# Kernel optimization log

Hardware: AMD Instinct MI355X
Metric: run time of the kernel (lower is better)

Reference implementation:

```python
import jax, jax.numpy as jnp
import numpy as np

D = 768; H = 12; DH = 64; P = 16; G = 14; NP = 196; L = 197
LD = 4; GD = 12          # local / latent depths
RL = 12; RG = 8          # tokens merged per layer (total_merge // depth)
B = 8
EPS = 1e-6


def layernorm(x, g, b):
    mu = x.mean(-1, keepdims=True)
    v = ((x - mu) ** 2).mean(-1, keepdims=True)
    return (x - mu) / jnp.sqrt(v + EPS) * g + b


def attention(x, size, qkv_w, qkv_b, pw, pb):
    # proportional attention: logits += log(token size)
    Bn, N, _ = x.shape
    qkv = (x @ qkv_w + qkv_b).reshape(Bn, N, 3, H, DH)
    q, k, v = (qkv[:, :, i].transpose(0, 2, 1, 3) for i in range(3))  # bhnd
    logits = jnp.einsum('bhqd,bhkd->bhqk', q, k) * (DH ** -0.5)
    logits = logits + jnp.log(size)[:, None, None, :, 0]
    a = jax.nn.softmax(logits, axis=-1)
    o = jnp.einsum('bhqk,bhkd->bhqd', a, v).transpose(0, 2, 1, 3).reshape(Bn, N, D)
    return o @ pw + pb, k.mean(1)  # metric = mean key over heads


def tome_merge(x, size, metric, r, tok_map):
    # ToMe bipartite soft matching + weighted-average merge + source-map update
    Bn, N, _ = x.shape
    t1, t2 = (N + 1) // 2, N // 2
    m = metric / jnp.linalg.norm(metric, axis=-1, keepdims=True)
    scores = jnp.einsum('bid,bjd->bij', m[:, ::2], m[:, 1::2])
    scores = scores.at[:, 0, :].set(-jnp.inf)  # protect cls token
    node_max, node_idx = scores.max(-1), scores.argmax(-1).astype(jnp.int32)
    order = jnp.argsort(-node_max, axis=-1).astype(jnp.int32)
    src_idx = order[:, :r]
    unm_idx = jnp.sort(order[:, r:], axis=-1)  # cls stays first
    dst_idx = jnp.take_along_axis(node_idx, src_idx, axis=1)
    bi = jnp.arange(Bn)[:, None]

    def merge_sum(v):
        a, b = v[:, ::2], v[:, 1::2]
        unm = jnp.take_along_axis(a, unm_idx[..., None], axis=1)
        s = jnp.take_along_axis(a, src_idx[..., None], axis=1)
        b = b.at[bi, dst_idx].add(s)
        return jnp.concatenate([unm, b], axis=1)

    new_size = merge_sum(size)
    new_x = merge_sum(x * size) / new_size
    # per-step old->new index map, then compose with running source map
    pos_a = jnp.zeros((Bn, t1), jnp.int32)
    pos_a = pos_a.at[bi, unm_idx].set(jnp.arange(t1 - r, dtype=jnp.int32))
    pos_a = pos_a.at[bi, src_idx].set((t1 - r) + dst_idx)
    step = jnp.zeros((Bn, N), jnp.int32)
    step = step.at[:, ::2].set(pos_a)
    step = step.at[:, 1::2].set((t1 - r) + jnp.arange(t2, dtype=jnp.int32)[None])
    return new_x, new_size, jnp.take_along_axis(step, tok_map, axis=1)


def encode(x, size, tok_map, r, p):
    ln1g, ln1b, qw, qb, pw, pb, ln2g, ln2b, f1w, f1b, f2w, f2b = p
    for i in range(ln1g.shape[0]):
        a, metric = attention(layernorm(x, ln1g[i], ln1b[i]), size, qw[i], qb[i], pw[i], pb[i])
        x = x + a
        if r > 0:
            x, size, tok_map = tome_merge(x, size, metric, r, tok_map)
        h = layernorm(x, ln2g[i], ln2b[i])
        x = x + (jax.nn.gelu(h @ f1w[i] + f1b[i], approximate=False) @ f2w[i] + f2b[i])
    return x, size, tok_map


def setup_inputs() -> dict:
    key = jax.random.key(0)
    ks = iter(jax.random.split(key, 64))
    def w(shape):
        return jax.random.normal(next(ks), shape, jnp.float32) * 0.02
    def blocks(d, pre):
        return {pre + 'ln1g': jnp.ones((d, D)), pre + 'ln1b': jnp.zeros((d, D)),
                pre + 'qkv_w': w((d, D, 3 * D)), pre + 'qkv_b': jnp.zeros((d, 3 * D)),
                pre + 'proj_w': w((d, D, D)), pre + 'proj_b': jnp.zeros((d, D)),
                pre + 'ln2g': jnp.ones((d, D)), pre + 'ln2b': jnp.zeros((d, D)),
                pre + 'fc1w': w((d, D, 4 * D)), pre + 'fc1b': jnp.zeros((d, 4 * D)),
                pre + 'fc2w': w((d, 4 * D, D)), pre + 'fc2b': jnp.zeros((d, D))}
    inp = dict(x=jax.random.normal(next(ks), (B, 3, 224, 224), jnp.float32),
               patch_w=w((3 * P * P, D)), patch_b=jnp.zeros((D,)),
               cls_tok=w((1, 1, D)), pos_emb=w((1, L, D)),
               l_ng=jnp.ones((D,)), l_nb=jnp.zeros((D,)),
               g_ng=jnp.ones((D,)), g_nb=jnp.zeros((D,)),
               head_w=w((D, 10)), head_b=jnp.zeros((10,)))
    inp.update(blocks(LD, 'l_'))
    inp.update(blocks(GD, 'g_'))
    return inp


def reference(x, patch_w, patch_b, cls_tok, pos_emb,
              l_ln1g, l_ln1b, l_qkv_w, l_qkv_b, l_proj_w, l_proj_b,
              l_ln2g, l_ln2b, l_fc1w, l_fc1b, l_fc2w, l_fc2b, l_ng, l_nb,
              g_ln1g, g_ln1b, g_qkv_w, g_qkv_b, g_proj_w, g_proj_b,
              g_ln2g, g_ln2b, g_fc1w, g_fc1b, g_fc2w, g_fc2b, g_ng, g_nb,
              head_w, head_b):
    Bn = x.shape[0]
    # non-overlapping 16x16 patchify == conv stride 16
    patches = x.reshape(Bn, 3, G, P, G, P).transpose(0, 2, 4, 1, 3, 5).reshape(Bn, NP, 3 * P * P)
    t = patches @ patch_w + patch_b
    t = jnp.concatenate([jnp.broadcast_to(cls_tok, (Bn, 1, D)), t], axis=1) + pos_emb
    size = jnp.ones((Bn, L, 1), t.dtype)
    tmap = jnp.broadcast_to(jnp.arange(L, dtype=jnp.int32)[None], (Bn, L))  # token_map_for_dtem
    lp = (l_ln1g, l_ln1b, l_qkv_w, l_qkv_b, l_proj_w, l_proj_b, l_ln2g, l_ln2b, l_fc1w, l_fc1b, l_fc2w, l_fc2b)
    xl, size, tmap = encode(t, size, tmap, RL, lp)   # local encoder: 197 -> 149 tokens
    xl = layernorm(xl, l_ng, l_nb)
    N1 = xl.shape[1]
    smap = jnp.broadcast_to(jnp.arange(N1, dtype=jnp.int32)[None], (Bn, N1))  # latent source_map
    gp = (g_ln1g, g_ln1b, g_qkv_w, g_qkv_b, g_proj_w, g_proj_b, g_ln2g, g_ln2b, g_fc1w, g_fc1b, g_fc2w, g_fc2b)
    xg, size, smap = encode(xl, size, smap, RG, gp)  # latent encoder: 149 -> 53 tokens
    xg = layernorm(xg, g_ng, g_nb)
    xr = jnp.take_along_axis(xg, smap[..., None], axis=1)   # token_unmerge_from_map (ToMe)
    xf = jnp.take_along_axis(xr, tmap[..., None], axis=1)   # token_unmerge_from_map_for_dtem
    return xf[:, 0] @ head_w + head_b  # cls token -> logits (B, 10)
```

## Files before the change

kernel.cpp:

```cpp
#include <hip/hip_runtime.h>
#include <math.h>

#define NB 8
#define SD 768
#define NHEAD 12
#define LMAX 197
#define QBLK 32
#define KBLK 64

typedef __attribute__((ext_vector_type(8))) short bf16x8;
typedef __attribute__((ext_vector_type(4))) float f32x4;

static __device__ __forceinline__ float geluf(float x){
    return 0.5f*x*(1.0f+erff(x*0.70710678118654752440f));
}

static __device__ __forceinline__ void split_bf16(float v, ushort& h, ushort& l){
    uint u = __float_as_uint(v);
    uint hb = (u + 0x7FFFu + ((u>>16)&1u)) >> 16;
    h = (ushort)hb;
    float rem = v - __uint_as_float(hb<<16);
    uint u2 = __float_as_uint(rem);
    l = (ushort)((u2 + 0x7FFFu + ((u2>>16)&1u)) >> 16);
}

__global__ __launch_bounds__(256) void wconv(const float* __restrict__ W,
        ushort* __restrict__ Hi, ushort* __restrict__ Lo, int K, int Nc)
{
    __shared__ float tile[32][33];
    int z = blockIdx.z;
    const float* Wz = W + (size_t)z*K*Nc;
    ushort* Hz = Hi + (size_t)z*Nc*K;
    ushort* Lz = Lo + (size_t)z*Nc*K;
    int n0 = blockIdx.x*32, k0 = blockIdx.y*32;
    int tx = threadIdx.x&31, ty = threadIdx.x>>5;
    #pragma unroll
    for (int i=0;i<32;i+=8) tile[ty+i][tx] = Wz[(size_t)(k0+ty+i)*Nc + n0+tx];
    __syncthreads();
    #pragma unroll
    for (int i=0;i<32;i+=8){
        float v = tile[tx][ty+i];
        ushort h,l; split_bf16(v,h,l);
        size_t o = (size_t)(n0+ty+i)*K + k0+tx;
        Hz[o]=h; Lz[o]=l;
    }
}

template<int EPI>
__global__ __launch_bounds__(256) void gemm_mfma(const ushort* __restrict__ AHi,
        const ushort* __restrict__ ALo, const ushort* __restrict__ WHi,
        const ushort* __restrict__ WLo, const float* __restrict__ bias,
        const float* __restrict__ R, float* __restrict__ C,
        ushort* __restrict__ CHi, ushort* __restrict__ CLo,
        int M, int Nc, int K, int ntok)
{
    __shared__ ushort sAhi[64*64], sAlo[64*64], sBhi[64*64], sBlo[64*64];
    const int t = threadIdx.x;
    const int bx = blockIdx.x, by = blockIdx.y;
    const int w = t>>6, l = t&63, lr = l&15, lg = l>>4;
    const int wr = w>>1, wc = w&1;
    const int srow = t>>3;
    const int kbyte = (t&7)*16;

    f32x4 acc[2][2];
    #pragma unroll
    for (int i=0;i<2;i++)
        #pragma unroll
        for (int j=0;j<2;j++) acc[i][j] = (f32x4){0.f,0.f,0.f,0.f};

    for (int k0=0;k0<K;k0+=64){
        #pragma unroll
        for (int p=0;p<2;p++){
            int row = p*32 + srow;
            int ar = by*64 + row; if (ar >= M) ar = M-1;
            int b = ar/ntok; int n = ar - b*ntok;
            size_t ga = ((size_t)(b*LMAX+n)*K + k0)*2 + kbyte;
            uint4 vah = *(const uint4*)((const char*)AHi + ga);
            uint4 val = *(const uint4*)((const char*)ALo + ga);
            uint off = (uint)((row*128 + kbyte) ^ ((row&7)<<4));
            *(uint4*)((char*)sAhi + off) = vah;
            *(uint4*)((char*)sAlo + off) = val;
            size_t gw = ((size_t)(bx*64+row)*K + k0)*2 + kbyte;
            uint4 vwh = *(const uint4*)((const char*)WHi + gw);
            uint4 vwl = *(const uint4*)((const char*)WLo + gw);
            *(uint4*)((char*)sBhi + off) = vwh;
            *(uint4*)((char*)sBlo + off) = vwl;
        }
        __syncthreads();
        #pragma unroll
        for (int kk=0;kk<2;kk++){
            bf16x8 ah[2], al[2], bh[2], bl[2];
            #pragma unroll
            for (int m=0;m<2;m++){
                int row = wr*32 + m*16 + lr;
                uint off = (uint)((row*128 + kk*64 + lg*16) ^ ((row&7)<<4));
                ah[m] = *(bf16x8*)((char*)sAhi + off);
                al[m] = *(bf16x8*)((char*)sAlo + off);
            }
            #pragma unroll
            for (int n=0;n<2;n++){
                int col = wc*32 + n*16 + lr;
                uint off = (uint)((col*128 + kk*64 + lg*16) ^ ((col&7)<<4));
                bh[n] = *(bf16x8*)((char*)sBhi + off);
                bl[n] = *(bf16x8*)((char*)sBlo + off);
            }
            #pragma unroll
            for (int m=0;m<2;m++)
                #pragma unroll
                for (int n=0;n<2;n++){
                    acc[m][n] = __builtin_amdgcn_mfma_f32_16x16x32_bf16(ah[m], bh[n], acc[m][n], 0,0,0);
                    acc[m][n] = __builtin_amdgcn_mfma_f32_16x16x32_bf16(ah[m], bl[n], acc[m][n], 0,0,0);
                    acc[m][n] = __builtin_amdgcn_mfma_f32_16x16x32_bf16(al[m], bh[n], acc[m][n], 0,0,0);
                }
        }
        __syncthreads();
    }
    #pragma unroll
    for (int m=0;m<2;m++){
        #pragma unroll
        for (int n=0;n<2;n++){
            int gcol = bx*64 + wc*32 + n*16 + lr;
            float bv = bias[gcol];
            #pragma unroll
            for (int r=0;r<4;r++){
                int grow = by*64 + wr*32 + m*16 + lg*4 + r;
                if (grow >= M) continue;
                int b = grow/ntok; int ni = grow - b*ntok;
                size_t off = (size_t)(b*LMAX+ni)*Nc + gcol;
                float v = acc[m][n][r] + bv;
                if (EPI==1){
                    v = geluf(v);
                    ushort h,lo; split_bf16(v,h,lo);
                    CHi[off]=h; CLo[off]=lo;
                } else {
                    if (EPI==2) v += R[off];
                    C[off] = v;
                }
            }
        }
    }
}

__device__ __forceinline__ float block_sum256(float v){
    __shared__ float red[4];
    for (int o=32;o>0;o>>=1) v += __shfl_down(v,o,64);
    int t=threadIdx.x;
    if ((t&63)==0) red[t>>6]=v;
    __syncthreads();
    float r = red[0]+red[1]+red[2]+red[3];
    __syncthreads();
    return r;
}

__global__ __launch_bounds__(256) void ln_split(const float* __restrict__ X,
        const float* __restrict__ gam, const float* __restrict__ bet,
        ushort* __restrict__ YHi, ushort* __restrict__ YLo)
{
    int n = blockIdx.x, b = blockIdx.y, t = threadIdx.x;
    const float* xr = X + ((size_t)(b*LMAX+n))*SD;
    size_t ro = ((size_t)(b*LMAX+n))*SD;
    float v0=xr[t], v1=xr[t+256], v2=xr[t+512];
    float mu = block_sum256(v0+v1+v2) * (1.0f/768.0f);
    float d0=v0-mu, d1=v1-mu, d2=v2-mu;
    float var = block_sum256(d0*d0+d1*d1+d2*d2) * (1.0f/768.0f);
    float rs = rsqrtf(var + 1e-6f);
    float y0 = d0*rs*gam[t]     + bet[t];
    float y1 = d1*rs*gam[t+256] + bet[t+256];
    float y2 = d2*rs*gam[t+512] + bet[t+512];
    ushort h,lo;
    split_bf16(y0,h,lo); YHi[ro+t]=h;     YLo[ro+t]=lo;
    split_bf16(y1,h,lo); YHi[ro+t+256]=h; YLo[ro+t+256]=lo;
    split_bf16(y2,h,lo); YHi[ro+t+512]=h; YLo[ro+t+512]=lo;
}

__global__ __launch_bounds__(256) void ln_kernel(const float* __restrict__ X,
        const float* __restrict__ gam, const float* __restrict__ bet,
        float* __restrict__ Y)
{
    int n = blockIdx.x, b = blockIdx.y, t = threadIdx.x;
    const float* xr = X + ((size_t)(b*LMAX+n))*SD;
    float* yr = Y + ((size_t)(b*LMAX+n))*SD;
    float v0=xr[t], v1=xr[t+256], v2=xr[t+512];
    float mu = block_sum256(v0+v1+v2) * (1.0f/768.0f);
    float d0=v0-mu, d1=v1-mu, d2=v2-mu;
    float var = block_sum256(d0*d0+d1*d1+d2*d2) * (1.0f/768.0f);
    float rs = rsqrtf(var + 1e-6f);
    yr[t]     = d0*rs*gam[t]     + bet[t];
    yr[t+256] = d1*rs*gam[t+256] + bet[t+256];
    yr[t+512] = d2*rs*gam[t+512] + bet[t+512];
}

__global__ __launch_bounds__(256) void attn_tile(const float* __restrict__ QKV,
        const float* __restrict__ SZ, ushort* __restrict__ OHi,
        ushort* __restrict__ OLo, int N)
{
    const int q0 = blockIdx.x*QBLK;
    const int h = blockIdx.y, b = blockIdx.z, t = threadIdx.x;
    __shared__ float Qs[QBLK][68];
    __shared__ float KVs[KBLK][68];
    __shared__ float Ls[QBLK][200];
    __shared__ float szl[KBLK];
    __shared__ float invs[QBLK];

    {
        int row = t>>3, seg = t&7;
        int q = q0 + row;
        if (q < N){
            const float* src = QKV + ((size_t)(b*LMAX+q))*2304 + h*64 + seg*8;
            *(float4*)&Qs[row][seg*8]   = *(const float4*)src;
            *(float4*)&Qs[row][seg*8+4] = *(const float4*)(src+4);
        } else {
            float4 z = make_float4(0.f,0.f,0.f,0.f);
            *(float4*)&Qs[row][seg*8]   = z;
            *(float4*)&Qs[row][seg*8+4] = z;
        }
    }
    const int tq = t>>3, tk = t&7;
    const int nkt = (N+KBLK-1)/KBLK;

    for (int kt=0; kt<nkt; ++kt){
        int kbase = kt*KBLK;
        __syncthreads();
        {
            int row = t>>2, seg = t&3;
            int ktok = kbase + row;
            float4 a,b4,c,d4;
            if (ktok < N){
                const float* src = QKV + ((size_t)(b*LMAX+ktok))*2304 + 768 + h*64 + seg*16;
                a=*(const float4*)src; b4=*(const float4*)(src+4);
                c=*(const float4*)(src+8); d4=*(const float4*)(src+12);
            } else {
                a=b4=c=d4=make_float4(0.f,0.f,0.f,0.f);
            }
            *(float4*)&KVs[row][seg*16]   =a;
            *(float4*)&KVs[row][seg*16+4] =b4;
            *(float4*)&KVs[row][seg*16+8] =c;
            *(float4*)&KVs[row][seg*16+12]=d4;
            if (t < KBLK){
                int kk2 = kbase + t;
                szl[t] = (kk2<N) ? logf(SZ[b*LMAX+kk2]) : 0.f;
            }
        }
        __syncthreads();
        float acc[8];
        #pragma unroll
        for (int j=0;j<8;j++) acc[j]=0.f;
        #pragma unroll 4
        for (int d4=0; d4<16; ++d4){
            float4 qv = *(const float4*)&Qs[tq][d4*4];
            #pragma unroll
            for (int j=0;j<8;j++){
                float4 kv = *(const float4*)&KVs[tk+8*j][d4*4];
                acc[j] += qv.x*kv.x + qv.y*kv.y + qv.z*kv.z + qv.w*kv.w;
            }
        }
        #pragma unroll
        for (int j=0;j<8;j++){
            int kk = kbase + tk + 8*j;
            if (kk < N) Ls[tq][kk] = acc[j]*0.125f + szl[tk+8*j];
        }
    }
    __syncthreads();

    {
        float m = -INFINITY;
        for (int k=tk;k<N;k+=8) m = fmaxf(m, Ls[tq][k]);
        #pragma unroll
        for (int o=1;o<8;o<<=1) m = fmaxf(m, __shfl_xor(m,o,64));
        float s = 0.f;
        for (int k=tk;k<N;k+=8){
            float p = expf(Ls[tq][k]-m);
            Ls[tq][k]=p; s+=p;
        }
        #pragma unroll
        for (int o=1;o<8;o<<=1) s += __shfl_xor(s,o,64);
        if (tk==0) invs[tq] = 1.0f/s;
    }

    float o0[8];
    #pragma unroll
    for (int i=0;i<8;i++) o0[i]=0.f;
    for (int kt=0; kt<nkt; ++kt){
        int kbase = kt*KBLK;
        __syncthreads();
        {
            int row = t>>2, seg = t&3;
            int ktok = kbase + row;
            float4 a,b4,c,d4;
            if (ktok < N){
                const float* src = QKV + ((size_t)(b*LMAX+ktok))*2304 + 1536 + h*64 + seg*16;
                a=*(const float4*)src; b4=*(const float4*)(src+4);
                c=*(const float4*)(src+8); d4=*(const float4*)(src+12);
            } else {
                a=b4=c=d4=make_float4(0.f,0.f,0.f,0.f);
            }
            *(float4*)&KVs[row][seg*16]   =a;
            *(float4*)&KVs[row][seg*16+4] =b4;
            *(float4*)&KVs[row][seg*16+8] =c;
            *(float4*)&KVs[row][seg*16+12]=d4;
        }
        __syncthreads();
        int kmax = N - kbase; if (kmax > KBLK) kmax = KBLK;
        for (int kk=0; kk<kmax; ++kk){
            float p = Ls[tq][kbase+kk];
            float4 v0 = *(const float4*)&KVs[kk][tk*8];
            float4 v1 = *(const float4*)&KVs[kk][tk*8+4];
            o0[0]+=p*v0.x; o0[1]+=p*v0.y; o0[2]+=p*v0.z; o0[3]+=p*v0.w;
            o0[4]+=p*v1.x; o0[5]+=p*v1.y; o0[6]+=p*v1.z; o0[7]+=p*v1.w;
        }
    }
    int q = q0 + tq;
    if (q < N){
        float inv = invs[tq];
        ushort hh[8], ll[8];
        #pragma unroll
        for (int i=0;i<8;i++){ split_bf16(o0[i]*inv, hh[i], ll[i]); }
        size_t o = ((size_t)(b*LMAX+q))*SD + h*64 + tk*8;
        *(ushort4*)(OHi+o)   = make_ushort4(hh[0],hh[1],hh[2],hh[3]);
        *(ushort4*)(OHi+o+4) = make_ushort4(hh[4],hh[5],hh[6],hh[7]);
        *(ushort4*)(OLo+o)   = make_ushort4(ll[0],ll[1],ll[2],ll[3]);
        *(ushort4*)(OLo+o+4) = make_ushort4(ll[4],ll[5],ll[6],ll[7]);
    }
}

__global__ void metric_k(const float* __restrict__ QKV, float* __restrict__ MET)
{
    const int n = blockIdx.x, b = blockIdx.y, d = threadIdx.x;
    const float* base = QKV + ((size_t)(b*LMAX+n))*2304 + 768 + d;
    float s=0.f;
    #pragma unroll
    for (int h=0;h<12;h++) s += base[h*64];
    s *= (1.0f/12.0f);
    float sq = s*s;
    for (int o=32;o>0;o>>=1) sq += __shfl_down(sq,o,64);
    float nrm = sqrtf(__shfl(sq,0,64));
    MET[((size_t)(b*LMAX+n))*64 + d] = s/nrm;
}

__global__ __launch_bounds__(128) void scores_k(const float* __restrict__ MET,
        float* __restrict__ NMAX, int* __restrict__ NIDX, int t2)
{
    const int i = blockIdx.x, b = blockIdx.y, t = threadIdx.x;
    __shared__ float ma[64];
    __shared__ float vals[128];
    __shared__ int idxs[128];
    if (t<64) ma[t] = MET[((size_t)(b*LMAX+2*i))*64+t];
    __syncthreads();
    float val = -INFINITY;
    if (t<t2 && i>0){
        const float* mb = MET + ((size_t)(b*LMAX+2*t+1))*64;
        float dot=0.f;
        #pragma unroll 8
        for (int dd=0;dd<64;dd++) dot += ma[dd]*mb[dd];
        val = dot;
    }
    vals[t]=val; idxs[t]=t; __syncthreads();
    for (int s=64;s>0;s>>=1){
        if (t<s){
            float v2=vals[t+s], v1=vals[t]; int i2=idxs[t+s];
            if (v2>v1 || (v2==v1 && i2<idxs[t])){ vals[t]=v2; idxs[t]=i2; }
        }
        __syncthreads();
    }
    if (t==0){ NMAX[b*128+i]=vals[0]; NIDX[b*128+i]=idxs[0]; }
}

__global__ __launch_bounds__(128) void plan_k(const float* __restrict__ NMAX,
        const int* __restrict__ NIDX, int* __restrict__ SRC, int* __restrict__ DST,
        int* __restrict__ STEP, int* __restrict__ INV, int t1, int t2, int r)
{
    const int b = blockIdx.x, i = threadIdx.x;
    __shared__ float nm[128];
    __shared__ int issrc[128];
    nm[i] = (i<t1) ? NMAX[b*128+i] : INFINITY;
    __syncthreads();
    int rank=0, is=0, ni=0;
    if (i<t1){
        float m = nm[i];
        for (int j=0;j<t1;j++){ float a=nm[j]; if (a>m || (a==m && j<i)) rank++; }
        is = (rank<r) ? 1:0;
        ni = NIDX[b*128+i];
    }
    issrc[i]=is; __syncthreads();
    if (i<t1){
        if (is){ SRC[b*16+rank]=i; DST[b*16+rank]=ni; STEP[b*LMAX+2*i] = t1-r+ni; }
        else {
            int cnt=0;
            for (int j=0;j<i;j++) cnt += 1-issrc[j];
            STEP[b*LMAX+2*i]=cnt;
            INV[b*LMAX+cnt]=2*i;
        }
    }
    if (i<t2){ STEP[b*LMAX+2*i+1]=t1-r+i; INV[b*LMAX+(t1-r)+i]=2*i+1; }
}

__global__ __launch_bounds__(256) void merge_fused(const float* __restrict__ X,
        const float* __restrict__ SZ, const int* __restrict__ INV,
        const int* __restrict__ SRC, const int* __restrict__ DST,
        float* __restrict__ XO, float* __restrict__ SZO, int t1, int r)
{
    int p = blockIdx.x, b = blockIdx.y, t = threadIdx.x;
    int base = t1 - r;
    float acc0, acc1, acc2, snew;
    if (p < base){
        int tok = INV[b*LMAX+p];
        float s = SZ[b*LMAX+tok];
        const float* xr = X + (size_t)(b*LMAX+tok)*SD;
        acc0=xr[t]*s; acc1=xr[t+256]*s; acc2=xr[t+512]*s; snew=s;
    } else {
        int d = p - base;
        int tok = 2*d+1;
        float s = SZ[b*LMAX+tok];
        const float* xr = X + (size_t)(b*LMAX+tok)*SD;
        acc0=xr[t]*s; acc1=xr[t+256]*s; acc2=xr[t+512]*s; snew=s;
        for (int k=0;k<r;k++){
            if (DST[b*16+k]==d){
                int st = 2*SRC[b*16+k];
                float ss = SZ[b*LMAX+st];
                const float* xs = X + (size_t)(b*LMAX+st)*SD;
                acc0+=xs[t]*ss; acc1+=xs[t+256]*ss; acc2+=xs[t+512]*ss; snew+=ss;
            }
        }
    }
    float inv = 1.0f/snew;
    float* o = XO + (size_t)(b*LMAX+p)*SD;
    o[t]=acc0*inv; o[t+256]=acc1*inv; o[t+512]=acc2*inv;
    if (t==0) SZO[b*LMAX+p]=snew;
}

__global__ void map_upd(int* __restrict__ MAP, const int* __restrict__ STEP, int mlen)
{
    int i = blockIdx.x*256+threadIdx.x;
    if (i >= NB*mlen) return;
    int b=i/mlen, t=i-b*mlen;
    MAP[b*LMAX+t] = STEP[b*LMAX + MAP[b*LMAX+t]];
}

__global__ void patchify(const float* __restrict__ X, ushort* __restrict__ PHi,
        ushort* __restrict__ PLo)
{
    size_t i = (size_t)blockIdx.x*256 + threadIdx.x;
    if (i >= (size_t)NB*196*768) return;
    int f = i % 768; size_t q = i/768; int p = q % 196; int b = q/196;
    int c = f >> 8, py = (f>>4)&15, px = f&15;
    int gy = p/14, gx = p - gy*14;
    float v = X[(((size_t)b*3 + c)*224 + gy*16+py)*224 + gx*16+px];
    ushort h,l; split_bf16(v,h,l);
    size_t o = ((size_t)(b*LMAX+p))*768 + f;
    PHi[o]=h; PLo[o]=l;
}

__global__ void assemble(const float* __restrict__ T, const float* __restrict__ cls,
        const float* __restrict__ pos, float* __restrict__ Xo)
{
    size_t i = (size_t)blockIdx.x*256 + threadIdx.x;
    if (i >= (size_t)NB*LMAX*768) return;
    int d = i % 768; size_t q = i/768; int n = q % LMAX; int b = q/LMAX;
    float v = (n==0) ? cls[d] : T[((size_t)(b*LMAX+n-1))*768+d];
    Xo[((size_t)(b*LMAX+n))*768+d] = v + pos[n*768+d];
}

__global__ void init_state(float* __restrict__ SZ, int* __restrict__ TMAP, int* __restrict__ SMAP)
{
    int i = blockIdx.x*256+threadIdx.x;
    if (i >= NB*LMAX) return;
    SZ[i]=1.0f;
    int n=i%LMAX;
    TMAP[i]=n;
    if (n<149) SMAP[i]=n;
}

__global__ void head_k(const float* __restrict__ XG, const int* __restrict__ SMAP,
        const int* __restrict__ TMAP, const float* __restrict__ HW,
        const float* __restrict__ HB, float* __restrict__ OUT)
{
    int t = threadIdx.x;
    if (t>=80) return;
    int b=t/10, o=t-b*10;
    int row = SMAP[b*LMAX + TMAP[b*LMAX]];
    const float* xr = XG + ((size_t)(b*LMAX+row))*SD;
    float acc = HB[o];
    for (int d=0;d<SD;d++) acc += xr[d]*HW[d*10+o];
    OUT[b*10+o]=acc;
}

extern "C" void kernel_launch(void* const* d_in, const int* in_sizes, int n_in,
                              void* d_out, int out_size, void* d_ws, size_t ws_size,
                              hipStream_t stream)
{
    const float* x_in    = (const float*)d_in[0];
    const float* patch_w = (const float*)d_in[1];
    const float* patch_b = (const float*)d_in[2];
    const float* cls     = (const float*)d_in[3];
    const float* pos     = (const float*)d_in[4];
    const float* l_ng    = (const float*)d_in[5];
    const float* l_nb    = (const float*)d_in[6];
    const float* g_ng    = (const float*)d_in[7];
    const float* g_nb    = (const float*)d_in[8];
    const float* head_w  = (const float*)d_in[9];
    const float* head_b  = (const float*)d_in[10];
    const float* L[12];  for (int i=0;i<12;i++) L[i]  = (const float*)d_in[11+i];
    const float* Gp[12]; for (int i=0;i<12;i++) Gp[i] = (const float*)d_in[23+i];
    float* out = (float*)d_out;

    float* fp = (float*)d_ws;
    float* xA      = fp; fp += (size_t)NB*LMAX*SD;
    float* xB      = fp; fp += (size_t)NB*LMAX*SD;
    float* qkvbuf  = fp; fp += (size_t)NB*LMAX*2304;
    float* metricbuf=fp; fp += (size_t)NB*LMAX*64;
    float* szA     = fp; fp += NB*LMAX;
    float* szB     = fp; fp += NB*LMAX;
    float* nodemax = fp; fp += NB*128;
    int* ip = (int*)fp;
    int* tmap    = ip; ip += NB*LMAX;
    int* smap    = ip; ip += NB*LMAX;
    int* stepbuf = ip; ip += NB*LMAX;
    int* invrow  = ip; ip += NB*LMAX;
    int* nodeidx = ip; ip += NB*128;
    int* srcs    = ip; ip += NB*16;
    int* dsts    = ip; ip += NB*16;
    uintptr_t up = ((uintptr_t)ip + 15) & ~(uintptr_t)15;
    ushort* sp = (ushort*)up;
    ushort* lnHi = sp; sp += (size_t)NB*LMAX*SD;
    ushort* lnLo = sp; sp += (size_t)NB*LMAX*SD;
    ushort* oHi  = sp; sp += (size_t)NB*LMAX*SD;
    ushort* oLo  = sp; sp += (size_t)NB*LMAX*SD;
    ushort* hHi  = sp; sp += (size_t)NB*LMAX*3072;
    ushort* hLo  = sp; sp += (size_t)NB*LMAX*3072;
    ushort* pHi  = sp; sp += (size_t)NB*LMAX*SD;
    ushort* pLo  = sp; sp += (size_t)NB*LMAX*SD;
    ushort* patchHi = sp; sp += (size_t)768*768;
    ushort* patchLo = sp; sp += (size_t)768*768;
    ushort* qkvHi = sp; sp += (size_t)4*768*2304;
    ushort* qkvLo = sp; sp += (size_t)4*768*2304;
    ushort* projHi= sp; sp += (size_t)4*768*768;
    ushort* projLo= sp; sp += (size_t)4*768*768;
    ushort* fc1Hi = sp; sp += (size_t)4*768*3072;
    ushort* fc1Lo = sp; sp += (size_t)4*768*3072;
    ushort* fc2Hi = sp; sp += (size_t)4*3072*768;
    ushort* fc2Lo = sp; sp += (size_t)4*3072*768;

    float *xc = xA, *xn = xB, *szc = szA, *szn = szB;

    auto conv_chunk = [&](const float* qw, const float* pw, const float* f1w,
                          const float* f2w, int nz)
    {
        wconv<<<dim3(2304/32,768/32,nz),256,0,stream>>>(qw, qkvHi, qkvLo, SD, 2304);
        wconv<<<dim3(768/32,768/32,nz),256,0,stream>>>(pw, projHi, projLo, SD, SD);
        wconv<<<dim3(3072/32,768/32,nz),256,0,stream>>>(f1w, fc1Hi, fc1Lo, SD, 3072);
        wconv<<<dim3(768/32,3072/32,nz),256,0,stream>>>(f2w, fc2Hi, fc2Lo, 3072, SD);
    };

    auto run_block = [&](const float* ln1g, const float* ln1b, const float* qb,
                         const float* pb, const float* ln2g, const float* ln2b,
                         const float* f1b, const float* f2b,
                         int slot, int N, int r, int* mp, int mlen)
    {
        int M = NB*N;
        const ushort* qH = qkvHi + (size_t)slot*768*2304;
        const ushort* qL = qkvLo + (size_t)slot*768*2304;
        const ushort* pH = projHi + (size_t)slot*768*768;
        const ushort* pL = projLo + (size_t)slot*768*768;
        const ushort* f1H = fc1Hi + (size_t)slot*768*3072;
        const ushort* f1L = fc1Lo + (size_t)slot*768*3072;
        const ushort* f2H = fc2Hi + (size_t)slot*3072*768;
        const ushort* f2L = fc2Lo + (size_t)slot*3072*768;

        ln_split<<<dim3(N,NB),256,0,stream>>>(xc, ln1g, ln1b, lnHi, lnLo);
        gemm_mfma<0><<<dim3(2304/64,(M+63)/64),256,0,stream>>>(lnHi, lnLo, qH, qL, qb, nullptr, qkvbuf, nullptr, nullptr, M, 2304, SD, N);
        attn_tile<<<dim3((N+QBLK-1)/QBLK,NHEAD,NB),256,0,stream>>>(qkvbuf, szc, oHi, oLo, N);
        metric_k<<<dim3(N,NB),64,0,stream>>>(qkvbuf, metricbuf);
        gemm_mfma<2><<<dim3(SD/64,(M+63)/64),256,0,stream>>>(oHi, oLo, pH, pL, pb, xc, xc, nullptr, nullptr, M, SD, SD, N);
        int t1=(N+1)/2, t2=N/2, Nn=N-r;
        scores_k<<<dim3(t1,NB),128,0,stream>>>(metricbuf, nodemax, nodeidx, t2);
        plan_k<<<NB,128,0,stream>>>(nodemax, nodeidx, srcs, dsts, stepbuf, invrow, t1, t2, r);
        merge_fused<<<dim3(Nn,NB),256,0,stream>>>(xc, szc, invrow, srcs, dsts, xn, szn, t1, r);
        map_upd<<<(NB*mlen+255)/256,256,0,stream>>>(mp, stepbuf, mlen);
        int M2 = NB*Nn;
        ln_split<<<dim3(Nn,NB),256,0,stream>>>(xn, ln2g, ln2b, lnHi, lnLo);
        gemm_mfma<1><<<dim3(3072/64,(M2+63)/64),256,0,stream>>>(lnHi, lnLo, f1H, f1L, f1b, nullptr, nullptr, hHi, hLo, M2, 3072, SD, Nn);
        gemm_mfma<2><<<dim3(SD/64,(M2+63)/64),256,0,stream>>>(hHi, hLo, f2H, f2L, f2b, xn, xn, nullptr, nullptr, M2, SD, 3072, Nn);
        float* tf; tf=xc; xc=xn; xn=tf; tf=szc; szc=szn; szn=tf;
    };

    {
        int tot = NB*196*768;
        patchify<<<(tot+255)/256,256,0,stream>>>(x_in, pHi, pLo);
        wconv<<<dim3(768/32,768/32,1),256,0,stream>>>(patch_w, patchHi, patchLo, SD, SD);
        gemm_mfma<0><<<dim3(SD/64,(NB*196+63)/64),256,0,stream>>>(pHi, pLo, patchHi, patchLo, patch_b, nullptr, qkvbuf, nullptr, nullptr, NB*196, SD, SD, 196);
        int tot2 = NB*LMAX*768;
        assemble<<<(tot2+255)/256,256,0,stream>>>(qkvbuf, cls, pos, xc);
        init_state<<<(NB*LMAX+255)/256,256,0,stream>>>(szc, tmap, smap);
    }

    conv_chunk(L[2], L[4], L[8], L[10], 4);
    int N = 197;
    for (int i=0;i<4;i++){
        run_block(L[0]+i*768, L[1]+i*768, L[3]+(size_t)i*2304,
                  L[5]+(size_t)i*768, L[6]+i*768, L[7]+i*768,
                  L[9]+(size_t)i*3072, L[11]+(size_t)i*768,
                  i, N, 12, tmap, 197);
        N -= 12;
    }
    ln_kernel<<<dim3(N,NB),256,0,stream>>>(xc, l_ng, l_nb, xc);

    for (int c=0;c<3;c++){
        conv_chunk(Gp[2]+(size_t)(4*c)*768*2304, Gp[4]+(size_t)(4*c)*768*768,
                   Gp[8]+(size_t)(4*c)*768*3072, Gp[10]+(size_t)(4*c)*3072*768, 4);
        for (int j=0;j<4;j++){
            int i = 4*c+j;
            run_block(Gp[0]+i*768, Gp[1]+i*768, Gp[3]+(size_t)i*2304,
                      Gp[5]+(size_t)i*768, Gp[6]+i*768, Gp[7]+i*768,
                      Gp[9]+(size_t)i*3072, Gp[11]+(size_t)i*768,
                      j, N, 8, smap, 149);
            N -= 8;
        }
    }
    ln_kernel<<<dim3(N,NB),256,0,stream>>>(xc, g_ng, g_nb, qkvbuf);
    head_k<<<1,128,0,stream>>>(qkvbuf, smap, tmap, head_w, head_b, out);
}
```

Measured before the change: 3.294 ms.

## Split-K the narrow projection and FC2 GEMMs and register-prefetch the next K tile

The proj and fc2 GEMMs, whose output is only 768 wide, now split K four ways across blockIdx.z. Each slice writes fp32 partials to a new workspace buffer, and a separate reduce kernel adds bias and the residual. This puts more blocks on the GPU for these small grids. All GEMMs also load the next K tile into registers while the current one is used, so global-load latency overlaps with MFMA work. The cost is extra partial-sum traffic, one more kernel launch per GEMM, and a change in summation order.

```diff
diff --git a/kernel.cpp b/kernel.cpp
--- a/kernel.cpp
+++ b/kernel.cpp
@@ -46,13 +46,13 @@
     }
 }
 
-template<int EPI>
+template<int EPI, int SPLITK>
 __global__ __launch_bounds__(256) void gemm_mfma(const ushort* __restrict__ AHi,
         const ushort* __restrict__ ALo, const ushort* __restrict__ WHi,
         const ushort* __restrict__ WLo, const float* __restrict__ bias,
         const float* __restrict__ R, float* __restrict__ C,
         ushort* __restrict__ CHi, ushort* __restrict__ CLo,
-        int M, int Nc, int K, int ntok)
+        float* __restrict__ Part, int M, int Nc, int K, int ntok)
 {
     __shared__ ushort sAhi[64*64], sAlo[64*64], sBhi[64*64], sBlo[64*64];
     const int t = threadIdx.x;
@@ -62,29 +62,53 @@
     const int srow = t>>3;
     const int kbyte = (t&7)*16;
 
+    const int Ks = K/SPLITK;
+    const int kbeg = blockIdx.z*Ks;
+
+    size_t gaB[2], gwB[2];
+    #pragma unroll
+    for (int p=0;p<2;p++){
+        int row = p*32 + srow;
+        int ar = by*64 + row; if (ar >= M) ar = M-1;
+        int b = ar/ntok; int n = ar - b*ntok;
+        gaB[p] = ((size_t)(b*LMAX+n)*K)*2 + kbyte;
+        gwB[p] = ((size_t)(bx*64+row)*K)*2 + kbyte;
+    }
+
+    uint4 rah[2], ral[2], rwh[2], rwl[2];
+    #pragma unroll
+    for (int p=0;p<2;p++){
+        rah[p] = *(const uint4*)((const char*)AHi + gaB[p] + (size_t)kbeg*2);
+        ral[p] = *(const uint4*)((const char*)ALo + gaB[p] + (size_t)kbeg*2);
+        rwh[p] = *(const uint4*)((const char*)WHi + gwB[p] + (size_t)kbeg*2);
+        rwl[p] = *(const uint4*)((const char*)WLo + gwB[p] + (size_t)kbeg*2);
+    }
+
     f32x4 acc[2][2];
     #pragma unroll
     for (int i=0;i<2;i++)
         #pragma unroll
         for (int j=0;j<2;j++) acc[i][j] = (f32x4){0.f,0.f,0.f,0.f};
 
-    for (int k0=0;k0<K;k0+=64){
+    for (int k0=kbeg; k0<kbeg+Ks; k0+=64){
         #pragma unroll
         for (int p=0;p<2;p++){
             int row = p*32 + srow;
-            int ar = by*64 + row; if (ar >= M) ar = M-1;
-            int b = ar/ntok; int n = ar - b*ntok;
-            size_t ga = ((size_t)(b*LMAX+n)*K + k0)*2 + kbyte;
-            uint4 vah = *(const uint4*)((const char*)AHi + ga);
-            uint4 val = *(const uint4*)((const char*)ALo + ga);
             uint off = (uint)((row*128 + kbyte) ^ ((row&7)<<4));
-            *(uint4*)((char*)sAhi + off) = vah;
-            *(uint4*)((char*)sAlo + off) = val;
-            size_t gw = ((size_t)(bx*64+row)*K + k0)*2 + kbyte;
-            uint4 vwh = *(const uint4*)((const char*)WHi + gw);
-            uint4 vwl = *(const uint4*)((const char*)WLo + gw);
-            *(uint4*)((char*)sBhi + off) = vwh;
-            *(uint4*)((char*)sBlo + off) = vwl;
+            *(uint4*)((char*)sAhi + off) = rah[p];
+            *(uint4*)((char*)sAlo + off) = ral[p];
+            *(uint4*)((char*)sBhi + off) = rwh[p];
+            *(uint4*)((char*)sBlo + off) = rwl[p];
+        }
+        if (k0+64 < kbeg+Ks){
+            size_t ko = (size_t)(k0+64)*2;
+            #pragma unroll
+            for (int p=0;p<2;p++){
+                rah[p] = *(const uint4*)((const char*)AHi + gaB[p] + ko);
+                ral[p] = *(const uint4*)((const char*)ALo + gaB[p] + ko);
+                rwh[p] = *(const uint4*)((const char*)WHi + gwB[p] + ko);
+                rwl[p] = *(const uint4*)((const char*)WLo + gwB[p] + ko);
+            }
         }
         __syncthreads();
         #pragma unroll
@@ -115,30 +139,71 @@
         }
         __syncthreads();
     }
-    #pragma unroll
-    for (int m=0;m<2;m++){
-        #pragma unroll
-        for (int n=0;n<2;n++){
-            int gcol = bx*64 + wc*32 + n*16 + lr;
-            float bv = bias[gcol];
+
+    if (SPLITK > 1){
+        float* Pz = Part + (size_t)blockIdx.z*M*Nc;
+        #pragma unroll
+        for (int m=0;m<2;m++){
             #pragma unroll
-            for (int r=0;r<4;r++){
-                int grow = by*64 + wr*32 + m*16 + lg*4 + r;
-                if (grow >= M) continue;
-                int b = grow/ntok; int ni = grow - b*ntok;
-                size_t off = (size_t)(b*LMAX+ni)*Nc + gcol;
-                float v = acc[m][n][r] + bv;
-                if (EPI==1){
-                    v = geluf(v);
-                    ushort h,lo; split_bf16(v,h,lo);
-                    CHi[off]=h; CLo[off]=lo;
-                } else {
-                    if (EPI==2) v += R[off];
-                    C[off] = v;
+            for (int n=0;n<2;n++){
+                int gcol = bx*64 + wc*32 + n*16 + lr;
+                #pragma unroll
+                for (int r=0;r<4;r++){
+                    int grow = by*64 + wr*32 + m*16 + lg*4 + r;
+                    if (grow >= M) continue;
+                    Pz[(size_t)grow*Nc + gcol] = acc[m][n][r];
                 }
             }
         }
-    }
+    } else {
+        #pragma unroll
+        for (int m=0;m<2;m++){
+            #pragma unroll
+            for (int n=0;n<2;n++){
+                int gcol = bx*64 + wc*32 + n*16 + lr;
+                float bv = bias[gcol];
+                #pragma unroll
+                for (int r=0;r<4;r++){
+                    int grow = by*64 + wr*32 + m*16 + lg*4 + r;
+                    if (grow >= M) continue;
+                    int b = grow/ntok; int ni = grow - b*ntok;
+                    size_t off = (size_t)(b*LMAX+ni)*Nc + gcol;
+                    float v = acc[m][n][r] + bv;
+                    if (EPI==1){
+                        v = geluf(v);
+                        ushort h,lo; split_bf16(v,h,lo);
+                        CHi[off]=h; CLo[off]=lo;
+                    } else {
+                        if (EPI==2) v += R[off];
+                        C[off] = v;
+                    }
+                }
+            }
+        }
+    }
+}
+
+__global__ __launch_bounds__(256) void reduce_k(const float* __restrict__ P,
+        const float* __restrict__ bias, const float* __restrict__ R,
+        float* __restrict__ C, int M, int Nc, int S, int ntok)
+{
+    int idx = blockIdx.x*256 + threadIdx.x;
+    int tot = M*(Nc/4);
+    if (idx >= tot) return;
+    int grow = idx/(Nc/4), c4 = idx - grow*(Nc/4);
+    size_t po = (size_t)grow*Nc + c4*4;
+    float4 a = *(const float4*)(P + po);
+    for (int s=1;s<S;s++){
+        float4 v = *(const float4*)(P + (size_t)s*M*Nc + po);
+        a.x+=v.x; a.y+=v.y; a.z+=v.z; a.w+=v.w;
+    }
+    int b = grow/ntok, n = grow - b*ntok;
+    size_t off = (size_t)(b*LMAX+n)*Nc + c4*4;
+    float4 bv = *(const float4*)(bias + c4*4);
+    float4 rv = *(const float4*)(R + off);
+    float4 o;
+    o.x=a.x+bv.x+rv.x; o.y=a.y+bv.y+rv.y; o.z=a.z+bv.z+rv.z; o.w=a.w+bv.w+rv.w;
+    *(float4*)(C + off) = o;
 }
 
 __device__ __forceinline__ float block_sum256(float v){
@@ -508,6 +573,7 @@
     float* xB      = fp; fp += (size_t)NB*LMAX*SD;
     float* qkvbuf  = fp; fp += (size_t)NB*LMAX*2304;
     float* metricbuf=fp; fp += (size_t)NB*LMAX*64;
+    float* partbuf = fp; fp += (size_t)4*NB*LMAX*SD;
     float* szA     = fp; fp += NB*LMAX;
     float* szB     = fp; fp += NB*LMAX;
     float* nodemax = fp; fp += NB*128;
@@ -557,6 +623,7 @@
                          int slot, int N, int r, int* mp, int mlen)
     {
         int M = NB*N;
+        int Mt = (M+63)/64;
         const ushort* qH = qkvHi + (size_t)slot*768*2304;
         const ushort* qL = qkvLo + (size_t)slot*768*2304;
         const ushort* pH = projHi + (size_t)slot*768*768;
@@ -567,19 +634,22 @@
         const ushort* f2L = fc2Lo + (size_t)slot*3072*768;
 
         ln_split<<<dim3(N,NB),256,0,stream>>>(xc, ln1g, ln1b, lnHi, lnLo);
-        gemm_mfma<0><<<dim3(2304/64,(M+63)/64),256,0,stream>>>(lnHi, lnLo, qH, qL, qb, nullptr, qkvbuf, nullptr, nullptr, M, 2304, SD, N);
+        gemm_mfma<0,1><<<dim3(2304/64,Mt),256,0,stream>>>(lnHi, lnLo, qH, qL, qb, nullptr, qkvbuf, nullptr, nullptr, nullptr, M, 2304, SD, N);
         attn_tile<<<dim3((N+QBLK-1)/QBLK,NHEAD,NB),256,0,stream>>>(qkvbuf, szc, oHi, oLo, N);
         metric_k<<<dim3(N,NB),64,0,stream>>>(qkvbuf, metricbuf);
-        gemm_mfma<2><<<dim3(SD/64,(M+63)/64),256,0,stream>>>(oHi, oLo, pH, pL, pb, xc, xc, nullptr, nullptr, M, SD, SD, N);
+        gemm_mfma<0,4><<<dim3(SD/64,Mt,4),256,0,stream>>>(oHi, oLo, pH, pL, nullptr, nullptr, nullptr, nullptr, nullptr, partbuf, M, SD, SD, N);
+        reduce_k<<<(M*(SD/4)+255)/256,256,0,stream>>>(partbuf, pb, xc, xc, M, SD, 4, N);
         int t1=(N+1)/2, t2=N/2, Nn=N-r;
         scores_k<<<dim3(t1,NB),128,0,stream>>>(metricbuf, nodemax, nodeidx, t2);
         plan_k<<<NB,128,0,stream>>>(nodemax, nodeidx, srcs, dsts, stepbuf, invrow, t1, t2, r);
         merge_fused<<<dim3(Nn,NB),256,0,stream>>>(xc, szc, invrow, srcs, dsts, xn, szn, t1, r);
         map_upd<<<(NB*mlen+255)/256,256,0,stream>>>(mp, stepbuf, mlen);
         int M2 = NB*Nn;
+        int M2t = (M2+63)/64;
         ln_split<<<dim3(Nn,NB),256,0,stream>>>(xn, ln2g, ln2b, lnHi, lnLo);
-        gemm_mfma<1><<<dim3(3072/64,(M2+63)/64),256,0,stream>>>(lnHi, lnLo, f1H, f1L, f1b, nullptr, nullptr, hHi, hLo, M2, 3072, SD, Nn);
-        gemm_mfma<2><<<dim3(SD/64,(M2+63)/64),256,0,stream>>>(hHi, hLo, f2H, f2L, f2b, xn, xn, nullptr, nullptr, M2, SD, 3072, Nn);
+        gemm_mfma<1,1><<<dim3(3072/64,M2t),256,0,stream>>>(lnHi, lnLo, f1H, f1L, f1b, nullptr, nullptr, hHi, hLo, nullptr, M2, 3072, SD, Nn);
+        gemm_mfma<0,4><<<dim3(SD/64,M2t,4),256,0,stream>>>(hHi, hLo, f2H, f2L, nullptr, nullptr, nullptr, nullptr, nullptr, partbuf, M2, SD, 3072, Nn);
+        reduce_k<<<(M2*(SD/4)+255)/256,256,0,stream>>>(partbuf, f2b, xn, xn, M2, SD, 4, Nn);
         float* tf; tf=xc; xc=xn; xn=tf; tf=szc; szc=szn; szn=tf;
     };
 
@@ -587,7 +657,7 @@
         int tot = NB*196*768;
         patchify<<<(tot+255)/256,256,0,stream>>>(x_in, pHi, pLo);
         wconv<<<dim3(768/32,768/32,1),256,0,stream>>>(patch_w, patchHi, patchLo, SD, SD);
-        gemm_mfma<0><<<dim3(SD/64,(NB*196+63)/64),256,0,stream>>>(pHi, pLo, patchHi, patchLo, patch_b, nullptr, qkvbuf, nullptr, nullptr, NB*196, SD, SD, 196);
+        gemm_mfma<0,1><<<dim3(SD/64,(NB*196+63)/64),256,0,stream>>>(pHi, pLo, patchHi, patchLo, patch_b, nullptr, qkvbuf, nullptr, nullptr, nullptr, NB*196, SD, SD, 196);
         int tot2 = NB*LMAX*768;
         assemble<<<(tot2+255)/256,256,0,stream>>>(qkvbuf, cls, pos, xc);
         init_state<<<(NB*LMAX+255)/256,256,0,stream>>>(szc, tmap, smap);
```

After: 6.808 ms. 107% more time.

## Double-buffer GEMM LDS tiles using direct global-to-LDS async loads

Applied to the files above, without the earlier changes.

The split-bf16 MFMA GEMM now keeps two LDS buffers per operand and issues global_load_lds for the next K tile while computing on the current one, so loads no longer pass through registers. The XOR swizzle moves to the global-side address, since each lane's chunk lands at a fixed LDS slot, and the per-row base pointers are hoisted out of the K loop. This is meant to hide global memory latency behind the MFMAs. In exchange it doubles shared memory per block, which may lower occupancy, and it depends on the swizzle mapping matching exactly.

```diff
diff --git a/kernel.cpp b/kernel.cpp
--- a/kernel.cpp
+++ b/kernel.cpp
@@ -10,6 +10,8 @@
 
 typedef __attribute__((ext_vector_type(8))) short bf16x8;
 typedef __attribute__((ext_vector_type(4))) float f32x4;
+typedef const __attribute__((address_space(1))) unsigned int gu32_t;
+typedef __attribute__((address_space(3))) unsigned int lu32_t;
 
 static __device__ __forceinline__ float geluf(float x){
     return 0.5f*x*(1.0f+erff(x*0.70710678118654752440f));
@@ -54,13 +56,25 @@
         ushort* __restrict__ CHi, ushort* __restrict__ CLo,
         int M, int Nc, int K, int ntok)
 {
-    __shared__ ushort sAhi[64*64], sAlo[64*64], sBhi[64*64], sBlo[64*64];
+    __shared__ ushort sAhi[2][4096], sAlo[2][4096], sBhi[2][4096], sBlo[2][4096];
     const int t = threadIdx.x;
     const int bx = blockIdx.x, by = blockIdx.y;
     const int w = t>>6, l = t&63, lr = l&15, lg = l>>4;
     const int wr = w>>1, wc = w&1;
     const int srow = t>>3;
-    const int kbyte = (t&7)*16;
+    const uint kchunk = (uint)(((l&7) ^ (l>>3)) << 4);
+
+    const char* pA[2][2]; const char* pW[2][2];
+    #pragma unroll
+    for (int p=0;p<2;p++){
+        int row = p*32 + srow;
+        int ar = by*64 + row; if (ar >= M) ar = M-1;
+        int b = ar/ntok; int n = ar - b*ntok;
+        size_t ab = ((size_t)(b*LMAX+n)*K)*2 + kchunk;
+        size_t wb = ((size_t)(bx*64+row)*K)*2 + kchunk;
+        pA[p][0] = (const char*)AHi + ab;  pA[p][1] = (const char*)ALo + ab;
+        pW[p][0] = (const char*)WHi + wb;  pW[p][1] = (const char*)WLo + wb;
+    }
 
     f32x4 acc[2][2];
     #pragma unroll
@@ -68,25 +82,31 @@
         #pragma unroll
         for (int j=0;j<2;j++) acc[i][j] = (f32x4){0.f,0.f,0.f,0.f};
 
-    for (int k0=0;k0<K;k0+=64){
+    const int nt = K/64;
+    int buf = 0;
+
+    auto stage = [&](int bf, int kt){
+        size_t ko = (size_t)kt*128;
         #pragma unroll
         for (int p=0;p<2;p++){
-            int row = p*32 + srow;
-            int ar = by*64 + row; if (ar >= M) ar = M-1;
-            int b = ar/ntok; int n = ar - b*ntok;
-            size_t ga = ((size_t)(b*LMAX+n)*K + k0)*2 + kbyte;
-            uint4 vah = *(const uint4*)((const char*)AHi + ga);
-            uint4 val = *(const uint4*)((const char*)ALo + ga);
-            uint off = (uint)((row*128 + kbyte) ^ ((row&7)<<4));
-            *(uint4*)((char*)sAhi + off) = vah;
-            *(uint4*)((char*)sAlo + off) = val;
-            size_t gw = ((size_t)(bx*64+row)*K + k0)*2 + kbyte;
-            uint4 vwh = *(const uint4*)((const char*)WHi + gw);
-            uint4 vwl = *(const uint4*)((const char*)WLo + gw);
-            *(uint4*)((char*)sBhi + off) = vwh;
-            *(uint4*)((char*)sBlo + off) = vwl;
-        }
-        __syncthreads();
+            uint lb = (uint)((p*32 + w*8)*64);
+            __builtin_amdgcn_global_load_lds((gu32_t*)(pA[p][0]+ko), (lu32_t*)&sAhi[bf][lb], 16, 0, 0);
+            __builtin_amdgcn_global_load_lds((gu32_t*)(pA[p][1]+ko), (lu32_t*)&sAlo[bf][lb], 16, 0, 0);
+            __builtin_amdgcn_global_load_lds((gu32_t*)(pW[p][0]+ko), (lu32_t*)&sBhi[bf][lb], 16, 0, 0);
+            __builtin_amdgcn_global_load_lds((gu32_t*)(pW[p][1]+ko), (lu32_t*)&sBlo[bf][lb], 16, 0, 0);
+        }
+    };
+
+    stage(0, 0);
+    asm volatile("s_waitcnt vmcnt(0)" ::: "memory");
+    __builtin_amdgcn_s_barrier();
+
+    for (int kt=0; kt<nt; ++kt){
+        if (kt+1 < nt) stage(buf^1, kt+1);
+        const char* bAhi = (const char*)&sAhi[buf][0];
+        const char* bAlo = (const char*)&sAlo[buf][0];
+        const char* bBhi = (const char*)&sBhi[buf][0];
+        const char* bBlo = (const char*)&sBlo[buf][0];
         #pragma unroll
         for (int kk=0;kk<2;kk++){
             bf16x8 ah[2], al[2], bh[2], bl[2];
@@ -94,15 +114,15 @@
             for (int m=0;m<2;m++){
                 int row = wr*32 + m*16 + lr;
                 uint off = (uint)((row*128 + kk*64 + lg*16) ^ ((row&7)<<4));
-                ah[m] = *(bf16x8*)((char*)sAhi + off);
-                al[m] = *(bf16x8*)((char*)sAlo + off);
+                ah[m] = *(const bf16x8*)(bAhi + off);
+                al[m] = *(const bf16x8*)(bAlo + off);
             }
             #pragma unroll
             for (int n=0;n<2;n++){
                 int col = wc*32 + n*16 + lr;
                 uint off = (uint)((col*128 + kk*64 + lg*16) ^ ((col&7)<<4));
-                bh[n] = *(bf16x8*)((char*)sBhi + off);
-                bl[n] = *(bf16x8*)((char*)sBlo + off);
+                bh[n] = *(const bf16x8*)(bBhi + off);
+                bl[n] = *(const bf16x8*)(bBlo + off);
             }
             #pragma unroll
             for (int m=0;m<2;m++)
@@ -113,8 +133,11 @@
                     acc[m][n] = __builtin_amdgcn_mfma_f32_16x16x32_bf16(al[m], bh[n], acc[m][n], 0,0,0);
                 }
         }
-        __syncthreads();
-    }
+        asm volatile("s_waitcnt vmcnt(0)" ::: "memory");
+        __builtin_amdgcn_s_barrier();
+        buf ^= 1;
+    }
+
     #pragma unroll
     for (int m=0;m<2;m++){
         #pragma unroll
@@ -557,6 +580,7 @@
                          int slot, int N, int r, int* mp, int mlen)
     {
         int M = NB*N;
+        int Mt = (M+63)/64;
         const ushort* qH = qkvHi + (size_t)slot*768*2304;
         const ushort* qL = qkvLo + (size_t)slot*768*2304;
         const ushort* pH = projHi + (size_t)slot*768*768;
@@ -567,19 +591,20 @@
         const ushort* f2L = fc2Lo + (size_t)slot*3072*768;
 
         ln_split<<<dim3(N,NB),256,0,stream>>>(xc, ln1g, ln1b, lnHi, lnLo);
-        gemm_mfma<0><<<dim3(2304/64,(M+63)/64),256,0,stream>>>(lnHi, lnLo, qH, qL, qb, nullptr, qkvbuf, nullptr, nullptr, M, 2304, SD, N);
+        gemm_mfma<0><<<dim3(2304/64,Mt),256,0,stream>>>(lnHi, lnLo, qH, qL, qb, nullptr, qkvbuf, nullptr, nullptr, M, 2304, SD, N);
         attn_tile<<<dim3((N+QBLK-1)/QBLK,NHEAD,NB),256,0,stream>>>(qkvbuf, szc, oHi, oLo, N);
         metric_k<<<dim3(N,NB),64,0,stream>>>(qkvbuf, metricbuf);
-        gemm_mfma<2><<<dim3(SD/64,(M+63)/64),256,0,stream>>>(oHi, oLo, pH, pL, pb, xc, xc, nullptr, nullptr, M, SD, SD, N);
+        gemm_mfma<2><<<dim3(SD/64,Mt),256,0,stream>>>(oHi, oLo, pH, pL, pb, xc, xc, nullptr, nullptr, M, SD, SD, N);
         int t1=(N+1)/2, t2=N/2, Nn=N-r;
         scores_k<<<dim3(t1,NB),128,0,stream>>>(metricbuf, nodemax, nodeidx, t2);
         plan_k<<<NB,128,0,stream>>>(nodemax, nodeidx, srcs, dsts, stepbuf, invrow, t1, t2, r);
         merge_fused<<<dim3(Nn,NB),256,0,stream>>>(xc, szc, invrow, srcs, dsts, xn, szn, t1, r);
         map_upd<<<(NB*mlen+255)/256,256,0,stream>>>(mp, stepbuf, mlen);
         int M2 = NB*Nn;
+        int M2t = (M2+63)/64;
         ln_split<<<dim3(Nn,NB),256,0,stream>>>(xn, ln2g, ln2b, lnHi, lnLo);
-        gemm_mfma<1><<<dim3(3072/64,(M2+63)/64),256,0,stream>>>(lnHi, lnLo, f1H, f1L, f1b, nullptr, nullptr, hHi, hLo, M2, 3072, SD, Nn);
-        gemm_mfma<2><<<dim3(SD/64,(M2+63)/64),256,0,stream>>>(hHi, hLo, f2H, f2L, f2b, xn, xn, nullptr, nullptr, M2, SD, 3072, Nn);
+        gemm_mfma<1><<<dim3(3072/64,M2t),256,0,stream>>>(lnHi, lnLo, f1H, f1L, f1b, nullptr, nullptr, hHi, hLo, M2, 3072, SD, Nn);
+        gemm_mfma<2><<<dim3(SD/64,M2t),256,0,stream>>>(hHi, hLo, f2H, f2L, f2b, xn, xn, nullptr, nullptr, M2, SD, 3072, Nn);
         float* tf; tf=xc; xc=xn; xn=tf; tf=szc; szc=szn; szn=tf;
     };
 
```

Measured after the change: 3.433 ms. 1.04x slower.
